# Optimization experiments

Measured on AMD Instinct MI355X. Metric: run time of the kernel, lower is better.

The kernel has to match this reference:

```python
import jax, jax.numpy as jnp
import numpy as np

N = 2048
VOTE_THRESH = 0.65
SOFT_TH = 0.05      # INFERENCE_TH in the original
MAX_DET = 100       # cfg.TEST.DETECTIONS_PER_IMAGE
NUM_CLASSES = 80


def setup_inputs() -> dict:
    key = jax.random.key(0)
    k1, k2, k3, k4 = jax.random.split(key, 4)
    xy = jax.random.uniform(k1, (N, 2), dtype=jnp.float32) * 800.0
    wh = jax.random.uniform(k2, (N, 2), dtype=jnp.float32) * 196.0 + 4.0
    boxes = jnp.concatenate([xy, xy + wh], axis=1)          # valid x1y1x2y2 boxes
    scores = jax.random.uniform(k3, (N,), dtype=jnp.float32) * 0.95 + 0.05
    labels = jax.random.randint(k4, (N,), 0, NUM_CLASSES, dtype=jnp.int32)
    return {"boxes": boxes, "scores": scores, "labels": labels}


def _bbox_vote_soft(det):
    """Faithful fixed-shape version of bbox_vote(..., vote_type='soft_vote').
    det: (n, 6) = [x1, y1, x2, y2, score, label]. Returns (MAX_DET, 6) rows + valid mask."""
    n = det.shape[0]
    BUF = 2 * n + 1                      # each det yields <=1 soft row + <=1 merged row; last slot = trash
    order = jnp.argsort(-det[:, 4])
    det = det[order]
    area = (det[:, 2] - det[:, 0]) * (det[:, 3] - det[:, 1])

    def step(state, _):
        alive, buf, cnt = state
        any_alive = jnp.any(alive)
        pos = jnp.argmax(alive)          # first alive in score-sorted order == current top det
        cur = det[pos]
        xx1 = jnp.maximum(cur[0], det[:, 0])
        yy1 = jnp.maximum(cur[1], det[:, 1])
        xx2 = jnp.minimum(cur[2], det[:, 2])
        yy2 = jnp.minimum(cur[3], det[:, 3])
        inter = jnp.clip(xx2 - xx1, 0.0) * jnp.clip(yy2 - yy1, 0.0)
        iou = inter / (area[pos] + area - inter)
        merge = alive & (iou >= VOTE_THRESH)
        n_merge = merge.sum()
        s = det[:, 4]
        ms = jnp.where(merge, s, 0.0)
        wsum = ms.sum()
        wsafe = jnp.where(wsum > 0, wsum, 1.0)          # guard masked no-op iterations
        wbox = (det[:, :4] * ms[:, None]).sum(0) / wsafe  # score-weighted box merge
        maxs = jnp.max(ms)                               # max score among merged (scores > 0)
        row0 = jnp.concatenate([wbox, maxs[None], cur[5][None]])  # == single det when n_merge==1
        soft_s = s * (1.0 - iou)                         # soft-NMS decayed scores
        soft_valid = merge & (soft_s >= SOFT_TH) & (n_merge > 1)
        soft_rows = jnp.concatenate([det[:, :4], soft_s[:, None], det[:, 5:6]], axis=1)
        valid = jnp.concatenate([any_alive[None], soft_valid])
        rows = jnp.concatenate([row0[None], soft_rows], axis=0)   # (n+1, 6)
        idxs = jnp.where(valid, cnt + jnp.cumsum(valid) - 1, BUF - 1)
        buf = buf.at[idxs].set(rows)
        cnt = cnt + valid.sum()
        alive = alive & (iou < VOTE_THRESH)              # drop all merged dets
        return (alive, buf, cnt), None

    init = (jnp.ones((n,), bool), jnp.zeros((BUF, 6), det.dtype), jnp.int32(0))
    (alive, buf, cnt), _ = jax.lax.scan(step, init, None, length=n)
    res = buf[: BUF - 1]
    valid = jnp.arange(BUF - 1) < cnt
    sc = jnp.where(valid, res[:, 4], -jnp.inf)
    keep = jnp.argsort(-sc)[:MAX_DET]                    # final sort by score desc + truncate
    return res[keep], valid[keep]


def reference(boxes, scores, labels):
    labf = labels.astype(boxes.dtype)
    maxc = boxes.max() + 1.0                             # batched-NMS class-offset trick
    det = jnp.concatenate([boxes + labf[:, None] * maxc, scores[:, None], labf[:, None]], axis=1)
    out, valid = _bbox_vote_soft(det)
    ob = jnp.where(valid[:, None], out[:, :4] - out[:, 5:6] * maxc, 0.0)
    os_ = jnp.where(valid, out[:, 4], 0.0)
    ol = jnp.where(valid, out[:, 5], 0.0)
    return ob, os_, ol
```

## Files before the change

kernel.cpp:

```cpp
#include <hip/hip_runtime.h>

#define NCLS 80
#define VOTE_TH 0.65f
#define SOFT_THR 0.05f
#define ROWCAP 2048
#define MAXDET 100
#define NBINS 5121
#define BINBASE 0x1E800
#define CANDCAP 1024

__device__ __forceinline__ int bin_of(unsigned int b) {
    int bin = (int)(b >> 13) - BINBASE;
    if (bin < 0) bin = 0;
    if (bin > NBINS - 1) bin = NBINS - 1;
    return bin;
}

__global__ __launch_bounds__(1024) void setup_kernel(
    const float* __restrict__ boxes,
    const float* __restrict__ scores,
    const int* __restrict__ labels,
    int* __restrict__ idxArr,
    float* __restrict__ scoreLst,
    int* __restrict__ kArr,
    float* __restrict__ maxcP,
    int* __restrict__ rowcnt,
    int n)
{
    const int tid = threadIdx.x;
    const int lane = tid & 63;
    const int wave = tid >> 6;
    const int chunks = (n + 63) >> 6;

    __shared__ int counts[32][NCLS];
    __shared__ float redmax[16];

    const float4* b4 = (const float4*)boxes;
    float m = -3.0e38f;
    for (int i = tid; i < n; i += 1024) {
        float4 v = b4[i];
        m = fmaxf(m, fmaxf(fmaxf(v.x, v.y), fmaxf(v.z, v.w)));
    }
#pragma unroll
    for (int d = 32; d; d >>= 1) m = fmaxf(m, __shfl_xor(m, d));
    if (lane == 0) redmax[wave] = m;

    for (int i = tid; i < 32 * NCLS; i += 1024) ((int*)counts)[i] = 0;
    __syncthreads();
    if (tid == 0) {
        float mm = redmax[0];
        for (int w = 1; w < 16; ++w) mm = fmaxf(mm, redmax[w]);
        *maxcP = mm + 1.0f;
        *rowcnt = 0;
    }

    int Ls[2] = {-1, -1}, ranks[2] = {0, 0}, gis[2] = {0, 0};
    for (int cc = 0; cc < 2; ++cc) {
        int c = wave + cc * 16;
        if (c >= chunks) break;
        int gi = c * 64 + lane;
        int L = (gi < n) ? labels[gi] : -1;
        int rank = 0, total = 0;
#pragma unroll
        for (int j = 0; j < 64; ++j) {
            int Lj = __shfl(L, j);
            bool e = (Lj == L);
            rank += (e && j < lane) ? 1 : 0;
            total += e ? 1 : 0;
        }
        if (L >= 0 && rank == total - 1) counts[c][L] = total;
        Ls[cc] = L; ranks[cc] = rank; gis[cc] = gi;
    }
    __syncthreads();

    if (tid < NCLS) {
        int running = 0;
#pragma unroll
        for (int c = 0; c < 32; ++c) {
            int t = counts[c][tid];
            counts[c][tid] = running;
            running += t;
        }
        kArr[tid] = (running > 64) ? 64 : running;
    }
    __syncthreads();

    for (int cc = 0; cc < 2; ++cc) {
        int c = wave + cc * 16;
        if (c >= chunks) break;
        int L = Ls[cc];
        if (L >= 0) {
            int pos = counts[c][L] + ranks[cc];
            if (pos < 64) {
                idxArr[L * 64 + pos] = gis[cc];
                scoreLst[L * 64 + pos] = scores[gis[cc]];
            }
        }
    }
}

__global__ __launch_bounds__(64) void vote_kernel(
    const float* __restrict__ boxes,
    const int* __restrict__ idxArr,
    const float* __restrict__ scoreLst,
    const int* __restrict__ kArr,
    const float* __restrict__ maxcP,
    float* __restrict__ rows,
    float* __restrict__ scoreArr,
    int* __restrict__ rowcnt)
{
#pragma clang fp contract(off)
    const int lane = threadIdx.x;
    const int cls = blockIdx.x;
    const unsigned long long lmask = (1ull << lane) - 1ull;
    const int k = kArr[cls];
    const float maxc = *maxcP;
    const float off = (float)cls * maxc;
    const float cls_f = (float)cls;

    __shared__ float rowbuf[64 * 6];

    float s = 0.0f; int gi = 0;
    if (lane < k) {
        gi = idxArr[cls * 64 + lane];
        s  = scoreLst[cls * 64 + lane];
    }

    int r = 0;
#pragma unroll
    for (int j = 0; j < 64; ++j) {
        float sj = __shfl(s, j);
        r += ((sj > s) || (sj == s && j < lane)) ? 1 : 0;
    }

    float x1 = 0.f, y1 = 0.f, x2 = 0.f, y2 = 0.f;
    if (lane < k) {
        float4 bb = ((const float4*)boxes)[gi];
        x1 = bb.x + off; y1 = bb.y + off;
        x2 = bb.z + off; y2 = bb.w + off;
    }
    int addr = r * 4;
    x1 = __int_as_float(__builtin_amdgcn_ds_permute(addr, __float_as_int(x1)));
    y1 = __int_as_float(__builtin_amdgcn_ds_permute(addr, __float_as_int(y1)));
    x2 = __int_as_float(__builtin_amdgcn_ds_permute(addr, __float_as_int(x2)));
    y2 = __int_as_float(__builtin_amdgcn_ds_permute(addr, __float_as_int(y2)));
    s  = __int_as_float(__builtin_amdgcn_ds_permute(addr, __float_as_int(s)));

    float area = (x2 - x1) * (y2 - y1);
    bool alive = lane < k;

    int lcnt = 0;
    while (true) {
        unsigned long long avm = __ballot(alive);
        if (avm == 0ull) break;
        int pos = (int)__builtin_ctzll(avm);

        float cx1 = __shfl(x1, pos), cy1 = __shfl(y1, pos);
        float cx2 = __shfl(x2, pos), cy2 = __shfl(y2, pos);
        float carea = __shfl(area, pos), cs = __shfl(s, pos);

        float xx1 = fmaxf(cx1, x1), yy1 = fmaxf(cy1, y1);
        float xx2 = fminf(cx2, x2), yy2 = fminf(cy2, y2);
        float inter = fmaxf(xx2 - xx1, 0.0f) * fmaxf(yy2 - yy1, 0.0f);
        float iou = inter / ((carea + area) - inter);

        bool merge = alive && (iou >= VOTE_TH);
        unsigned long long mb = __ballot(merge);
        int nm = __popcll(mb);

        if (nm == 1) {
            if (lane == 0) {
                float* rp = rowbuf + lcnt * 6;
                rp[0] = (cx1 * cs) / cs; rp[1] = (cy1 * cs) / cs;
                rp[2] = (cx2 * cs) / cs; rp[3] = (cy2 * cs) / cs;
                rp[4] = cs; rp[5] = cls_f;
            }
            lcnt += 1;
        } else {
            float msv = merge ? s : 0.0f;
            float w0 = msv, w1 = x1 * msv, w2 = y1 * msv, w3 = x2 * msv, w4 = y2 * msv;
#pragma unroll
            for (int d = 32; d; d >>= 1) {
                w0 += __shfl_xor(w0, d);
                w1 += __shfl_xor(w1, d);
                w2 += __shfl_xor(w2, d);
                w3 += __shfl_xor(w3, d);
                w4 += __shfl_xor(w4, d);
            }
            float soft = s * (1.0f - iou);
            bool sv = merge && (soft >= SOFT_THR);
            unsigned long long sb = __ballot(sv);
            int nsoft = __popcll(sb);
            if (lane == 0) {
                float* rp = rowbuf + lcnt * 6;
                rp[0] = w1 / w0; rp[1] = w2 / w0;
                rp[2] = w3 / w0; rp[3] = w4 / w0;
                rp[4] = cs; rp[5] = cls_f;
            }
            if (sv) {
                int wp = lcnt + 1 + __popcll(sb & lmask);
                float* rp = rowbuf + wp * 6;
                rp[0] = x1; rp[1] = y1; rp[2] = x2; rp[3] = y2;
                rp[4] = soft; rp[5] = cls_f;
            }
            lcnt += 1 + nsoft;
        }
        alive = alive && (iou < VOTE_TH);
    }

    int slot = 0;
    if (lane == 0) slot = atomicAdd(rowcnt, lcnt);
    slot = __shfl(slot, 0);
    __syncthreads();
    for (int i = lane; i < lcnt * 6; i += 64) rows[slot * 6 + i] = rowbuf[i];
    for (int i = lane; i < lcnt; i += 64) scoreArr[slot + i] = rowbuf[i * 6 + 4];
}

__global__ __launch_bounds__(256) void select_kernel(
    const float* __restrict__ rows,
    const float* __restrict__ scoreArr,
    const int* __restrict__ rowcnt,
    const float* __restrict__ maxcPtr,
    float* __restrict__ out)
{
#pragma clang fp contract(off)
    const int tid = threadIdx.x;
    const int lane = tid & 63;
    __shared__ int hist[NBINS];
    __shared__ int chunkSum[21];
    __shared__ unsigned long long candKeys[CANDCAP];
    __shared__ int ncand, Jsh, carrySh, Tsh;

    int cnt = *rowcnt;
    if (cnt > ROWCAP) cnt = ROWCAP;
    if (cnt <= 0) return;
    const int K = (cnt < MAXDET) ? cnt : MAXDET;

    for (int i = tid; i < NBINS; i += 256) hist[i] = 0;
    if (tid == 0) { ncand = 0; Tsh = 0; }
    __syncthreads();

    for (int i = tid; i < cnt; i += 256)
        atomicAdd(&hist[bin_of(__float_as_uint(scoreArr[i]))], 1);
    __syncthreads();

    if (tid < 21) {
        int s = 0, base = tid * 256;
        int end = base + 256; if (end > NBINS) end = NBINS;
        for (int b = base; b < end; ++b) s += hist[b];
        chunkSum[tid] = s;
    }
    __syncthreads();

    if (tid < 64) {
        int suf = 0;
        if (tid < 21) for (int j = tid; j < 21; ++j) suf += chunkSum[j];
        unsigned long long bm = __ballot(tid < 21 && suf >= K);
        int J = 63 - __builtin_clzll(bm);
        if (tid == J) { Jsh = J; carrySh = suf - chunkSum[J]; }
    }
    __syncthreads();

    {
        int J = Jsh, carry = carrySh;
        int b = J * 256 + tid;
        if (b < NBINS) {
            int end = J * 256 + 256; if (end > NBINS) end = NBINS;
            int suf = carry;
            for (int bb = b; bb < end; ++bb) suf += hist[bb];
            if (suf >= K) atomicMax(&Tsh, b);
        }
    }
    __syncthreads();
    const int T = Tsh;

    for (int i = tid; i < cnt; i += 256) {
        unsigned int sb = __float_as_uint(scoreArr[i]);
        if (bin_of(sb) >= T) {
            int p = atomicAdd(&ncand, 1);
            if (p < CANDCAP)
                candKeys[p] = ((unsigned long long)sb << 32) |
                              (unsigned long long)(0xFFFFFFFFu - (unsigned int)i);
        }
    }
    __syncthreads();

    int nc = ncand; if (nc > CANDCAP) nc = CANDCAP;
    const float maxc = *maxcPtr;
    for (int j = tid; j < nc; j += 256) {
        unsigned long long my = candKeys[j];
        int rank = 0;
        for (int l = 0; l < nc; ++l) rank += (candKeys[l] > my) ? 1 : 0;
        if (rank < K) {
            int i = (int)(0xFFFFFFFFu - (unsigned int)(my & 0xFFFFFFFFull));
            const float* rp = rows + i * 6;
            float lb = rp[5];
            float o = lb * maxc;
            out[rank * 4 + 0] = rp[0] - o;
            out[rank * 4 + 1] = rp[1] - o;
            out[rank * 4 + 2] = rp[2] - o;
            out[rank * 4 + 3] = rp[3] - o;
            out[4 * MAXDET + rank] = rp[4];
            out[5 * MAXDET + rank] = lb;
        }
    }
}

extern "C" void kernel_launch(void* const* d_in, const int* in_sizes, int n_in,
                              void* d_out, int out_size, void* d_ws, size_t ws_size,
                              hipStream_t stream) {
    const float* boxes  = (const float*)d_in[0];
    const float* scores = (const float*)d_in[1];
    const int*   labels = (const int*)d_in[2];
    float* out = (float*)d_out;
    const int n = in_sizes[1];

    char* ws = (char*)d_ws;
    int*   rowcnt   = (int*)(ws + 0);
    float* maxcP    = (float*)(ws + 4);
    int*   kArr     = (int*)(ws + 64);
    int*   idxArr   = (int*)(ws + 512);
    float* scoreLst = (float*)(ws + 512 + 20480);
    float* rows     = (float*)(ws + 512 + 40960);
    float* scoreArr = (float*)(ws + 512 + 40960 + ROWCAP * 24);

    hipMemsetAsync(d_out, 0, out_size * sizeof(float), stream);
    hipLaunchKernelGGL(setup_kernel, dim3(1), dim3(1024), 0, stream,
                       boxes, scores, labels, idxArr, scoreLst, kArr, maxcP, rowcnt, n);
    hipLaunchKernelGGL(vote_kernel, dim3(NCLS), dim3(64), 0, stream,
                       boxes, idxArr, scoreLst, kArr, maxcP, rows, scoreArr, rowcnt);
    hipLaunchKernelGGL(select_kernel, dim3(1), dim3(256), 0, stream,
                       rows, scoreArr, rowcnt, maxcP, out);
}
```

Before: 104.0 us.

## Fuse setup, vote and select into a single-block kernel with LDS staging

Merges the three kernels and the output memset into one 1024-thread, single-block kernel. Per-class lists, the score array and the histogram now live in shared memory. Each of the 16 waves processes 5 classes in turn, and rows are allocated through a shared-memory atomic counter. The histogram is made coarser (1281 bins) and the candidate cap is halved. This removes launch and memset overhead and global round trips, but serialises the 80 class votes onto one CU.

```diff
diff --git a/kernel.cpp b/kernel.cpp
--- a/kernel.cpp
+++ b/kernel.cpp
@@ -5,35 +5,42 @@
 #define SOFT_THR 0.05f
 #define ROWCAP 2048
 #define MAXDET 100
-#define NBINS 5121
-#define BINBASE 0x1E800
-#define CANDCAP 1024
+#define NB 1281
+#define BINBASE 31232
+#define CANDCAP 512
+#define NCHUNK 6
 
 __device__ __forceinline__ int bin_of(unsigned int b) {
-    int bin = (int)(b >> 13) - BINBASE;
-    if (bin < 0) bin = 0;
-    if (bin > NBINS - 1) bin = NBINS - 1;
-    return bin;
+    int bin = (int)(b >> 15) - BINBASE;
+    return bin < 0 ? 0 : (bin > NB - 1 ? NB - 1 : bin);
 }
 
-__global__ __launch_bounds__(1024) void setup_kernel(
+__global__ __launch_bounds__(1024) void fused_kernel(
     const float* __restrict__ boxes,
     const float* __restrict__ scores,
     const int* __restrict__ labels,
-    int* __restrict__ idxArr,
-    float* __restrict__ scoreLst,
-    int* __restrict__ kArr,
-    float* __restrict__ maxcP,
-    int* __restrict__ rowcnt,
+    float* __restrict__ rows,
+    float* __restrict__ out,
     int n)
 {
+#pragma clang fp contract(off)
     const int tid = threadIdx.x;
     const int lane = tid & 63;
     const int wave = tid >> 6;
+    const unsigned long long lmask = (1ull << lane) - 1ull;
     const int chunks = (n + 63) >> 6;
 
-    __shared__ int counts[32][NCLS];
+    __shared__ int   idxL[NCLS * 64];
+    __shared__ float scoL[NCLS * 64];
+    __shared__ float sArr[ROWCAP];
+    __shared__ int   ubuf[2560];
+    __shared__ int   kSh[NCLS];
     __shared__ float redmax[16];
+    __shared__ float maxcSh;
+    __shared__ int   rowcntSh, ncand, Jsh, carrySh, Tsh;
+    __shared__ int   chunkSum[NCHUNK];
+
+    for (int i = tid; i < 6 * MAXDET; i += 1024) out[i] = 0.0f;
 
     const float4* b4 = (const float4*)boxes;
     float m = -3.0e38f;
@@ -45,13 +52,14 @@
     for (int d = 32; d; d >>= 1) m = fmaxf(m, __shfl_xor(m, d));
     if (lane == 0) redmax[wave] = m;
 
-    for (int i = tid; i < 32 * NCLS; i += 1024) ((int*)counts)[i] = 0;
+    int* counts = ubuf;
+    for (int i = tid; i < 32 * NCLS; i += 1024) counts[i] = 0;
     __syncthreads();
     if (tid == 0) {
         float mm = redmax[0];
         for (int w = 1; w < 16; ++w) mm = fmaxf(mm, redmax[w]);
-        *maxcP = mm + 1.0f;
-        *rowcnt = 0;
+        maxcSh = mm + 1.0f;
+        rowcntSh = 0; ncand = 0; Tsh = 0;
     }
 
     int Ls[2] = {-1, -1}, ranks[2] = {0, 0}, gis[2] = {0, 0};
@@ -68,7 +76,7 @@
             rank += (e && j < lane) ? 1 : 0;
             total += e ? 1 : 0;
         }
-        if (L >= 0 && rank == total - 1) counts[c][L] = total;
+        if (L >= 0 && rank == total - 1) counts[c * NCLS + L] = total;
         Ls[cc] = L; ranks[cc] = rank; gis[cc] = gi;
     }
     __syncthreads();
@@ -77,11 +85,11 @@
         int running = 0;
 #pragma unroll
         for (int c = 0; c < 32; ++c) {
-            int t = counts[c][tid];
-            counts[c][tid] = running;
+            int t = counts[c * NCLS + tid];
+            counts[c * NCLS + tid] = running;
             running += t;
         }
-        kArr[tid] = (running > 64) ? 64 : running;
+        kSh[tid] = (running > 64) ? 64 : running;
     }
     __syncthreads();
 
@@ -90,163 +98,135 @@
         if (c >= chunks) break;
         int L = Ls[cc];
         if (L >= 0) {
-            int pos = counts[c][L] + ranks[cc];
+            int pos = counts[c * NCLS + L] + ranks[cc];
             if (pos < 64) {
-                idxArr[L * 64 + pos] = gis[cc];
-                scoreLst[L * 64 + pos] = scores[gis[cc]];
+                idxL[L * 64 + pos] = gis[cc];
+                scoL[L * 64 + pos] = scores[gis[cc]];
             }
         }
     }
-}
-
-__global__ __launch_bounds__(64) void vote_kernel(
-    const float* __restrict__ boxes,
-    const int* __restrict__ idxArr,
-    const float* __restrict__ scoreLst,
-    const int* __restrict__ kArr,
-    const float* __restrict__ maxcP,
-    float* __restrict__ rows,
-    float* __restrict__ scoreArr,
-    int* __restrict__ rowcnt)
-{
-#pragma clang fp contract(off)
-    const int lane = threadIdx.x;
-    const int cls = blockIdx.x;
-    const unsigned long long lmask = (1ull << lane) - 1ull;
-    const int k = kArr[cls];
-    const float maxc = *maxcP;
-    const float off = (float)cls * maxc;
-    const float cls_f = (float)cls;
-
-    __shared__ float rowbuf[64 * 6];
-
-    float s = 0.0f; int gi = 0;
-    if (lane < k) {
-        gi = idxArr[cls * 64 + lane];
-        s  = scoreLst[cls * 64 + lane];
-    }
-
-    int r = 0;
-#pragma unroll
-    for (int j = 0; j < 64; ++j) {
-        float sj = __shfl(s, j);
-        r += ((sj > s) || (sj == s && j < lane)) ? 1 : 0;
-    }
-
-    float x1 = 0.f, y1 = 0.f, x2 = 0.f, y2 = 0.f;
-    if (lane < k) {
-        float4 bb = ((const float4*)boxes)[gi];
-        x1 = bb.x + off; y1 = bb.y + off;
-        x2 = bb.z + off; y2 = bb.w + off;
-    }
-    int addr = r * 4;
-    x1 = __int_as_float(__builtin_amdgcn_ds_permute(addr, __float_as_int(x1)));
-    y1 = __int_as_float(__builtin_amdgcn_ds_permute(addr, __float_as_int(y1)));
-    x2 = __int_as_float(__builtin_amdgcn_ds_permute(addr, __float_as_int(x2)));
-    y2 = __int_as_float(__builtin_amdgcn_ds_permute(addr, __float_as_int(y2)));
-    s  = __int_as_float(__builtin_amdgcn_ds_permute(addr, __float_as_int(s)));
-
-    float area = (x2 - x1) * (y2 - y1);
-    bool alive = lane < k;
-
-    int lcnt = 0;
-    while (true) {
-        unsigned long long avm = __ballot(alive);
-        if (avm == 0ull) break;
-        int pos = (int)__builtin_ctzll(avm);
-
-        float cx1 = __shfl(x1, pos), cy1 = __shfl(y1, pos);
-        float cx2 = __shfl(x2, pos), cy2 = __shfl(y2, pos);
-        float carea = __shfl(area, pos), cs = __shfl(s, pos);
-
-        float xx1 = fmaxf(cx1, x1), yy1 = fmaxf(cy1, y1);
-        float xx2 = fminf(cx2, x2), yy2 = fminf(cy2, y2);
-        float inter = fmaxf(xx2 - xx1, 0.0f) * fmaxf(yy2 - yy1, 0.0f);
-        float iou = inter / ((carea + area) - inter);
-
-        bool merge = alive && (iou >= VOTE_TH);
-        unsigned long long mb = __ballot(merge);
-        int nm = __popcll(mb);
-
-        if (nm == 1) {
-            if (lane == 0) {
-                float* rp = rowbuf + lcnt * 6;
-                rp[0] = (cx1 * cs) / cs; rp[1] = (cy1 * cs) / cs;
-                rp[2] = (cx2 * cs) / cs; rp[3] = (cy2 * cs) / cs;
-                rp[4] = cs; rp[5] = cls_f;
+    __syncthreads();
+
+    const float maxc = maxcSh;
+    for (int jj = 0; jj < 5; ++jj) {
+        const int cls = wave + 16 * jj;
+        const int k = kSh[cls];
+        const float off = (float)cls * maxc;
+        const float cls_f = (float)cls;
+
+        float s = 0.0f; int gi = 0;
+        if (lane < k) {
+            gi = idxL[cls * 64 + lane];
+            s  = scoL[cls * 64 + lane];
+        }
+        int r = 0;
+#pragma unroll
+        for (int j = 0; j < 64; ++j) {
+            float sj = __shfl(s, j);
+            r += ((sj > s) || (sj == s && j < lane)) ? 1 : 0;
+        }
+        float x1 = 0.f, y1 = 0.f, x2 = 0.f, y2 = 0.f;
+        if (lane < k) {
+            float4 bb = b4[gi];
+            x1 = bb.x + off; y1 = bb.y + off;
+            x2 = bb.z + off; y2 = bb.w + off;
+        }
+        int addr = r * 4;
+        x1 = __int_as_float(__builtin_amdgcn_ds_permute(addr, __float_as_int(x1)));
+        y1 = __int_as_float(__builtin_amdgcn_ds_permute(addr, __float_as_int(y1)));
+        x2 = __int_as_float(__builtin_amdgcn_ds_permute(addr, __float_as_int(x2)));
+        y2 = __int_as_float(__builtin_amdgcn_ds_permute(addr, __float_as_int(y2)));
+        s  = __int_as_float(__builtin_amdgcn_ds_permute(addr, __float_as_int(s)));
+
+        float area = (x2 - x1) * (y2 - y1);
+        bool alive = lane < k;
+
+        while (true) {
+            unsigned long long avm = __ballot(alive);
+            if (avm == 0ull) break;
+            int pos = (int)__builtin_ctzll(avm);
+
+            float cx1 = __shfl(x1, pos), cy1 = __shfl(y1, pos);
+            float cx2 = __shfl(x2, pos), cy2 = __shfl(y2, pos);
+            float carea = __shfl(area, pos), cs = __shfl(s, pos);
+
+            float xx1 = fmaxf(cx1, x1), yy1 = fmaxf(cy1, y1);
+            float xx2 = fminf(cx2, x2), yy2 = fminf(cy2, y2);
+            float inter = fmaxf(xx2 - xx1, 0.0f) * fmaxf(yy2 - yy1, 0.0f);
+            float iou = inter / ((carea + area) - inter);
+
+            bool merge = alive && (iou >= VOTE_TH);
+            unsigned long long mb = __ballot(merge);
+            int nm = __popcll(mb);
+
+            if (nm == 1) {
+                if (lane == 0) {
+                    int slot = atomicAdd(&rowcntSh, 1);
+                    if (slot < ROWCAP) {
+                        float* rp = rows + slot * 6;
+                        rp[0] = (cx1 * cs) / cs; rp[1] = (cy1 * cs) / cs;
+                        rp[2] = (cx2 * cs) / cs; rp[3] = (cy2 * cs) / cs;
+                        rp[4] = cs; rp[5] = cls_f;
+                        sArr[slot] = cs;
+                    }
+                }
+            } else {
+                float msv = merge ? s : 0.0f;
+                float w0 = msv, w1 = x1 * msv, w2 = y1 * msv, w3 = x2 * msv, w4 = y2 * msv;
+#pragma unroll
+                for (int d = 32; d; d >>= 1) {
+                    w0 += __shfl_xor(w0, d);
+                    w1 += __shfl_xor(w1, d);
+                    w2 += __shfl_xor(w2, d);
+                    w3 += __shfl_xor(w3, d);
+                    w4 += __shfl_xor(w4, d);
+                }
+                float soft = s * (1.0f - iou);
+                bool sv = merge && (soft >= SOFT_THR);
+                unsigned long long sb = __ballot(sv);
+                int nsoft = __popcll(sb);
+                int slot = 0;
+                if (lane == 0) slot = atomicAdd(&rowcntSh, 1 + nsoft);
+                slot = __shfl(slot, 0);
+                if (lane == 0 && slot < ROWCAP) {
+                    float* rp = rows + slot * 6;
+                    rp[0] = w1 / w0; rp[1] = w2 / w0;
+                    rp[2] = w3 / w0; rp[3] = w4 / w0;
+                    rp[4] = cs; rp[5] = cls_f;
+                    sArr[slot] = cs;
+                }
+                if (sv) {
+                    int wp = slot + 1 + __popcll(sb & lmask);
+                    if (wp < ROWCAP) {
+                        float* rp = rows + wp * 6;
+                        rp[0] = x1; rp[1] = y1; rp[2] = x2; rp[3] = y2;
+                        rp[4] = soft; rp[5] = cls_f;
+                        sArr[wp] = soft;
+                    }
+                }
             }
-            lcnt += 1;
-        } else {
-            float msv = merge ? s : 0.0f;
-            float w0 = msv, w1 = x1 * msv, w2 = y1 * msv, w3 = x2 * msv, w4 = y2 * msv;
-#pragma unroll
-            for (int d = 32; d; d >>= 1) {
-                w0 += __shfl_xor(w0, d);
-                w1 += __shfl_xor(w1, d);
-                w2 += __shfl_xor(w2, d);
-                w3 += __shfl_xor(w3, d);
-                w4 += __shfl_xor(w4, d);
-            }
-            float soft = s * (1.0f - iou);
-            bool sv = merge && (soft >= SOFT_THR);
-            unsigned long long sb = __ballot(sv);
-            int nsoft = __popcll(sb);
-            if (lane == 0) {
-                float* rp = rowbuf + lcnt * 6;
-                rp[0] = w1 / w0; rp[1] = w2 / w0;
-                rp[2] = w3 / w0; rp[3] = w4 / w0;
-                rp[4] = cs; rp[5] = cls_f;
-            }
-            if (sv) {
-                int wp = lcnt + 1 + __popcll(sb & lmask);
-                float* rp = rowbuf + wp * 6;
-                rp[0] = x1; rp[1] = y1; rp[2] = x2; rp[3] = y2;
-                rp[4] = soft; rp[5] = cls_f;
-            }
-            lcnt += 1 + nsoft;
-        }
-        alive = alive && (iou < VOTE_TH);
-    }
-
-    int slot = 0;
-    if (lane == 0) slot = atomicAdd(rowcnt, lcnt);
-    slot = __shfl(slot, 0);
-    __syncthreads();
-    for (int i = lane; i < lcnt * 6; i += 64) rows[slot * 6 + i] = rowbuf[i];
-    for (int i = lane; i < lcnt; i += 64) scoreArr[slot + i] = rowbuf[i * 6 + 4];
-}
-
-__global__ __launch_bounds__(256) void select_kernel(
-    const float* __restrict__ rows,
-    const float* __restrict__ scoreArr,
-    const int* __restrict__ rowcnt,
-    const float* __restrict__ maxcPtr,
-    float* __restrict__ out)
-{
-#pragma clang fp contract(off)
-    const int tid = threadIdx.x;
-    const int lane = tid & 63;
-    __shared__ int hist[NBINS];
-    __shared__ int chunkSum[21];
-    __shared__ unsigned long long candKeys[CANDCAP];
-    __shared__ int ncand, Jsh, carrySh, Tsh;
-
-    int cnt = *rowcnt;
+            alive = alive && (iou < VOTE_TH);
+        }
+    }
+    __syncthreads();
+
+    int cnt = rowcntSh;
     if (cnt > ROWCAP) cnt = ROWCAP;
     if (cnt <= 0) return;
     const int K = (cnt < MAXDET) ? cnt : MAXDET;
 
-    for (int i = tid; i < NBINS; i += 256) hist[i] = 0;
-    if (tid == 0) { ncand = 0; Tsh = 0; }
-    __syncthreads();
-
-    for (int i = tid; i < cnt; i += 256)
-        atomicAdd(&hist[bin_of(__float_as_uint(scoreArr[i]))], 1);
-    __syncthreads();
-
-    if (tid < 21) {
+    int* hist = ubuf;
+    unsigned long long* cand = (unsigned long long*)(ubuf + 1536);
+    for (int i = tid; i < NB; i += 1024) hist[i] = 0;
+    __syncthreads();
+
+    for (int i = tid; i < cnt; i += 1024)
+        atomicAdd(&hist[bin_of(__float_as_uint(sArr[i]))], 1);
+    __syncthreads();
+
+    if (tid < NCHUNK) {
         int s = 0, base = tid * 256;
-        int end = base + 256; if (end > NBINS) end = NBINS;
+        int end = base + 256; if (end > NB) end = NB;
         for (int b = base; b < end; ++b) s += hist[b];
         chunkSum[tid] = s;
     }
@@ -254,19 +234,18 @@
 
     if (tid < 64) {
         int suf = 0;
-        if (tid < 21) for (int j = tid; j < 21; ++j) suf += chunkSum[j];
-        unsigned long long bm = __ballot(tid < 21 && suf >= K);
+        if (tid < NCHUNK) for (int j = tid; j < NCHUNK; ++j) suf += chunkSum[j];
+        unsigned long long bm = __ballot(tid < NCHUNK && suf >= K);
         int J = 63 - __builtin_clzll(bm);
         if (tid == J) { Jsh = J; carrySh = suf - chunkSum[J]; }
     }
     __syncthreads();
 
-    {
-        int J = Jsh, carry = carrySh;
-        int b = J * 256 + tid;
-        if (b < NBINS) {
-            int end = J * 256 + 256; if (end > NBINS) end = NBINS;
-            int suf = carry;
+    if (tid < 256) {
+        int J = Jsh, b = J * 256 + tid;
+        if (b < NB) {
+            int end = J * 256 + 256; if (end > NB) end = NB;
+            int suf = carrySh;
             for (int bb = b; bb < end; ++bb) suf += hist[bb];
             if (suf >= K) atomicMax(&Tsh, b);
         }
@@ -274,23 +253,22 @@
     __syncthreads();
     const int T = Tsh;
 
-    for (int i = tid; i < cnt; i += 256) {
-        unsigned int sb = __float_as_uint(scoreArr[i]);
+    for (int i = tid; i < cnt; i += 1024) {
+        unsigned int sb = __float_as_uint(sArr[i]);
         if (bin_of(sb) >= T) {
             int p = atomicAdd(&ncand, 1);
             if (p < CANDCAP)
-                candKeys[p] = ((unsigned long long)sb << 32) |
-                              (unsigned long long)(0xFFFFFFFFu - (unsigned int)i);
+                cand[p] = ((unsigned long long)sb << 32) |
+                          (unsigned long long)(0xFFFFFFFFu - (unsigned int)i);
         }
     }
     __syncthreads();
 
     int nc = ncand; if (nc > CANDCAP) nc = CANDCAP;
-    const float maxc = *maxcPtr;
-    for (int j = tid; j < nc; j += 256) {
-        unsigned long long my = candKeys[j];
+    for (int j = tid; j < nc; j += 1024) {
+        unsigned long long my = cand[j];
         int rank = 0;
-        for (int l = 0; l < nc; ++l) rank += (candKeys[l] > my) ? 1 : 0;
+        for (int l = 0; l < nc; ++l) rank += (cand[l] > my) ? 1 : 0;
         if (rank < K) {
             int i = (int)(0xFFFFFFFFu - (unsigned int)(my & 0xFFFFFFFFull));
             const float* rp = rows + i * 6;
@@ -312,23 +290,10 @@
     const float* boxes  = (const float*)d_in[0];
     const float* scores = (const float*)d_in[1];
     const int*   labels = (const int*)d_in[2];
-    float* out = (float*)d_out;
+    float* out  = (float*)d_out;
+    float* rows = (float*)d_ws;
     const int n = in_sizes[1];
 
-    char* ws = (char*)d_ws;
-    int*   rowcnt   = (int*)(ws + 0);
-    float* maxcP    = (float*)(ws + 4);
-    int*   kArr     = (int*)(ws + 64);
-    int*   idxArr   = (int*)(ws + 512);
-    float* scoreLst = (float*)(ws + 512 + 20480);
-    float* rows     = (float*)(ws + 512 + 40960);
-    float* scoreArr = (float*)(ws + 512 + 40960 + ROWCAP * 24);
-
-    hipMemsetAsync(d_out, 0, out_size * sizeof(float), stream);
-    hipLaunchKernelGGL(setup_kernel, dim3(1), dim3(1024), 0, stream,
-                       boxes, scores, labels, idxArr, scoreLst, kArr, maxcP, rowcnt, n);
-    hipLaunchKernelGGL(vote_kernel, dim3(NCLS), dim3(64), 0, stream,
-                       boxes, idxArr, scoreLst, kArr, maxcP, rows, scoreArr, rowcnt);
-    hipLaunchKernelGGL(select_kernel, dim3(1), dim3(256), 0, stream,
-                       rows, scoreArr, rowcnt, maxcP, out);
+    hipLaunchKernelGGL(fused_kernel, dim3(1), dim3(1024), 0, stream,
+                       boxes, scores, labels, rows, out, n);
 }
```

After: 191.0 us. 83.6% more time.
